# Performance work log

Measured on AMD Instinct MI355X. Metric: run time of the kernel, lower is better.

## Reference

```python
import jax, jax.numpy as jnp
import numpy as np
import math

B, L, D, P, H, WIN, MAXLEN = 2, 2048, 256, 32, 4, 5, 16384


def setup_inputs() -> dict:
    key = jax.random.key(0)
    ks = iter(jax.random.split(key, 40))
    def w(shape, scale=0.05):
        return jax.random.normal(next(ks), shape, jnp.float32) * scale
    inp = {
        'x': jax.random.normal(next(ks), (B, L, D), jnp.float32),
        'pos_phases': jax.random.normal(next(ks), (MAXLEN, P), jnp.float32) * math.pi,
        # mem1_content_encoder
        'w_content': w((D, D)), 'b_content': jnp.zeros((D,), jnp.float32),
        # head_offset_predictors (stacked over H): Linear(D+P, D//2) -> GELU -> Linear(D//2, P+1)
        'hop_w1': w((H, D // 2, D + P)), 'hop_b1': jnp.zeros((H, D // 2), jnp.float32),
        'hop_w2': w((H, P + 1, D // 2)), 'hop_b2': jnp.zeros((H, P + 1), jnp.float32),
        # content_phase_encoder
        'w_cpe': w((P, D)), 'b_cpe': jnp.zeros((P,), jnp.float32),
        # value_encoder
        'w_val': w((D, D)), 'b_val': jnp.zeros((D,), jnp.float32),
        # kv_context_encoder
        'w_ctx': w((D, D)), 'b_ctx': jnp.zeros((D,), jnp.float32),
        # kv_storage_key: Linear(2D, D) -> GELU -> Linear(D, P)
        'kv_w1': w((D, 2 * D)), 'kv_b1': jnp.zeros((D,), jnp.float32),
        'kv_w2': w((P, D)), 'kv_b2': jnp.zeros((P,), jnp.float32),
        # store_gate: Linear(D, D//2) -> GELU -> Linear(D//2, 1) -> Sigmoid
        'sg_w1': w((D // 2, D)), 'sg_b1': jnp.zeros((D // 2,), jnp.float32),
        'sg_w2': w((1, D // 2)), 'sg_b2': jnp.zeros((1,), jnp.float32),
        # to_out: LayerNorm(D) -> Linear(D, D)
        'ln_g': jnp.ones((D,), jnp.float32), 'ln_b': jnp.zeros((D,), jnp.float32),
        'w_out': w((D, D)), 'b_out': jnp.zeros((D,), jnp.float32),
    }
    return inp


def reference(x, pos_phases, w_content, b_content, hop_w1, hop_b1, hop_w2, hop_b2,
              w_cpe, b_cpe, w_val, b_val, w_ctx, b_ctx, kv_w1, kv_b1, kv_w2, kv_b2,
              sg_w1, sg_b1, sg_w2, sg_b2, ln_g, ln_b, w_out, b_out):
    gelu = lambda t: jax.nn.gelu(t, approximate=False)  # torch exact GELU
    pp = pos_phases[:L]                      # (L,P)
    pos_cos, pos_sin = jnp.cos(pp), jnp.sin(pp)

    # ---- phasor memory 1: position-bound content cumsum ----
    content = x @ w_content.T + b_content    # (B,L,D)
    mem1_cos = jnp.cumsum(pos_cos[None, :, :, None] * content[:, :, None, :], axis=1)  # (B,L,P,D)
    mem1_sin = jnp.cumsum(pos_sin[None, :, :, None] * content[:, :, None, :], axis=1)

    # ---- per-head learned offsets ----
    offset_input = jnp.concatenate([x, jnp.broadcast_to(pp[None], (B, L, P))], axis=-1)  # (B,L,D+P)
    h1 = gelu(jnp.einsum('blf,hgf->bhlg', offset_input, hop_w1) + hop_b1[None, :, None, :])
    off = jnp.einsum('bhlg,hpg->bhlp', h1, hop_w2) + hop_b2[None, :, None, :]  # (B,H,L,P+1)
    center = jnp.tanh(off[..., :P]) * math.pi    # (B,H,L,P)
    ww = jax.nn.sigmoid(off[..., P:]) * 2 + 0.1  # (B,H,L,1)

    head_ret = jnp.zeros((B, H, L, D), x.dtype)
    tot_w = jnp.zeros((B, H, L, 1), x.dtype)
    half = WIN // 2
    for delta in range(-half, half + 1):
        wgt = jnp.exp(-0.5 * delta ** 2 / (ww ** 2 + 1e-6))
        op = center + delta * 0.1
        oc, os = jnp.cos(op), jnp.sin(op)
        qc = pos_cos[None, None] * oc - pos_sin[None, None] * os
        qs = pos_sin[None, None] * oc + pos_cos[None, None] * os
        ret = (jnp.einsum('blpd,bhlp->bhld', mem1_cos, qc)
               + jnp.einsum('blpd,bhlp->bhld', mem1_sin, qs)) / math.sqrt(P)
        head_ret = head_ret + wgt * ret
        tot_w = tot_w + wgt
    multi_head_out = (head_ret / (tot_w + 1e-6)).mean(axis=1)  # (B,L,D)

    # ---- kv phasor memory ----
    key_ph = jnp.tanh(x @ w_cpe.T + b_cpe) * math.pi            # (B,L,P)
    values = x @ w_val.T + b_val                                 # (B,L,D)
    store_gate = jax.nn.sigmoid(gelu(x @ sg_w1.T + sg_b1) @ sg_w2.T + sg_b2)  # (B,L,1)
    ctx = x @ w_ctx.T + b_ctx
    ctx_avg = jnp.cumsum(ctx, axis=1) / jnp.arange(1, L + 1, dtype=x.dtype)[None, :, None]
    storage_in = jnp.concatenate([x, ctx_avg], axis=-1)          # (B,L,2D)
    sp = jnp.tanh(gelu(storage_in @ kv_w1.T + kv_b1) @ kv_w2.T + kv_b2) * math.pi  # (B,L,P)
    gated_v = values * store_gate                                # (B,L,D)
    kv_cos = jnp.cumsum(jnp.cos(sp)[..., None] * gated_v[:, :, None, :], axis=1)  # (B,L,P,D)
    kv_sin = jnp.cumsum(jnp.sin(sp)[..., None] * gated_v[:, :, None, :], axis=1)
    gate_cum = jnp.clip(jnp.cumsum(store_gate, axis=1), 1.0, None)  # (B,L,1)
    kv_ret = (jnp.einsum('blpd,blp->bld', kv_cos, jnp.cos(key_ph))
              + jnp.einsum('blpd,blp->bld', kv_sin, jnp.sin(key_ph)))
    kv_ret = kv_ret / (jnp.sqrt(gate_cum) * math.sqrt(P))

    # ---- output projection ----
    combined = multi_head_out + kv_ret
    mu = combined.mean(-1, keepdims=True)
    var = combined.var(-1, keepdims=True)
    ln = (combined - mu) / jnp.sqrt(var + 1e-5) * ln_g + ln_b
    return x + ln @ w_out.T + b_out
```

## Files before the change

kernel.cpp:

```cpp
#include <hip/hip_runtime.h>
#include <hip/hip_bf16.h>

#define BB 2
#define LL 2048
#define DD 256
#define PP 32
#define PX 64
#define NROW (BB*LL)
#define COLS 1440
#define KIN 288
#define CC 64
#define NC (LL/CC)
#define PI_F 3.14159265358979323846f

typedef __attribute__((ext_vector_type(8))) short bf16x8;
typedef __attribute__((ext_vector_type(4))) float f32x4;

__device__ __forceinline__ float gelu_f(float v){
    return 0.5f*v*(1.0f+erff(v*0.70710678118654752440f));
}
__device__ __forceinline__ float sigm_f(float v){
    return 1.0f/(1.0f+expf(-v));
}
__device__ __forceinline__ short f2b(float v){
    __hip_bfloat16 h = __float2bfloat16(v);
    return *reinterpret_cast<short*>(&h);
}
__device__ __forceinline__ float b2f(unsigned short u){
    unsigned int x = ((unsigned int)u)<<16;
    return __uint_as_float(x);
}

__global__ void kprep(const float* w_content,const float* w_val,const float* w_ctx,
                      const float* w_cpe,const float* sg_w1,const float* hop_w1,
                      const float* b_content,const float* b_val,const float* b_ctx,
                      const float* b_cpe,const float* sg_b1,const float* hop_b1,
                      const float* pos_phases,const float* kv_w1,const float* kv_w2,
                      const float* hop_w2,const float* w_out,const float* x,
                      short* W_catb,float* bias_cat,float* w2mem,
                      short* kvw1b,short* kvw2b,float* hop_w2T,short* w_outb,
                      short* Xb,short* Xin2b){
    int idx = blockIdx.x*256 + threadIdx.x;
    int n1 = COLS*KIN;
    if (idx < n1){
        int row = idx / KIN, k = idx % KIN;
        float v = 0.f;
        if      (row < 256){ if (k<256) v = w_content[row*256+k]; }
        else if (row < 512){ if (k<256) v = w_val[(row-256)*256+k]; }
        else if (row < 768){ if (k<256) v = w_ctx[(row-512)*256+k]; }
        else if (row < 800){ if (k<256) v = w_cpe[(row-768)*256+k]; }
        else if (row < 928){ if (k<256) v = sg_w1[(row-800)*256+k]; }
        else               { v = hop_w1[(row-928)*288 + k]; }
        W_catb[idx] = f2b(v);
        return;
    }
    idx -= n1;
    if (idx < COLS){
        int row = idx; float v = 0.f;
        if      (row < 256) v = b_content[row];
        else if (row < 512) v = b_val[row-256];
        else if (row < 768) v = b_ctx[row-512];
        else if (row < 800) v = b_cpe[row-768];
        else if (row < 928) v = sg_b1[row-800];
        else                v = hop_b1[row-928];
        bias_cat[row] = v;
        return;
    }
    idx -= COLS;
    if (idx < LL*PP){
        int l = idx/PP, p = idx%PP;
        float ph = pos_phases[l*PP+p];
        w2mem[l*PX+p]     = cosf(ph);
        w2mem[l*PX+32+p]  = sinf(ph);
        return;
    }
    idx -= LL*PP;
    if (idx < 256*512){ kvw1b[idx] = f2b(kv_w1[idx]); return; }
    idx -= 256*512;
    if (idx < 32*256){ kvw2b[idx] = f2b(kv_w2[idx]); return; }
    idx -= 32*256;
    if (idx < 128*132){
        int k=idx/132, o=idx%132;
        hop_w2T[idx] = hop_w2[o*128+k];
        return;
    }
    idx -= 128*132;
    if (idx < 256*256){ w_outb[idx] = f2b(w_out[idx]); return; }
    idx -= 256*256;
    if (idx < NROW*KIN){
        int r = idx / KIN, d = idx % KIN;
        float v;
        if (d < 256){ v = x[(size_t)r*DD + d]; Xin2b[(size_t)r*512 + d] = f2b(v); }
        else          v = pos_phases[(r % LL)*PP + (d-256)];
        Xb[idx] = f2b(v);
    }
}

__global__ __launch_bounds__(256) void kA_gemm(const short* Xb,const short* Wb,short* Yb){
    int t=threadIdx.x;
    int wid=t>>6, l=t&63;
    int q=blockIdx.x;
    int ct=q%15, rt=q/15;
    int r0=rt*64 + wid*16;
    int c0=ct*96;
    int lr=l&15, lk=(l>>4)*8;
    const short* ap = Xb + (size_t)(r0+lr)*KIN + lk;
    const short* bp = Wb + (size_t)(c0+lr)*KIN + lk;
    f32x4 acc[6];
    #pragma unroll
    for (int f=0;f<6;f++) acc[f]=(f32x4){0.f,0.f,0.f,0.f};
    for (int ks=0;ks<9;ks++){
        bf16x8 a = *(const bf16x8*)(ap + ks*32);
        #pragma unroll
        for (int f=0;f<6;f++){
            bf16x8 b = *(const bf16x8*)(bp + (size_t)f*16*KIN + ks*32);
            acc[f] = __builtin_amdgcn_mfma_f32_16x16x32_bf16(a,b,acc[f],0,0,0);
        }
    }
    int orow = r0 + (l>>4)*4;
    int ocol = c0 + lr;
    #pragma unroll
    for (int f=0;f<6;f++){
        #pragma unroll
        for (int qq=0;qq<4;qq++){
            Yb[(size_t)(orow+qq)*COLS + ocol + 16*f] = f2b(acc[f][qq]);
        }
    }
}

__global__ __launch_bounds__(256,4) void kA_post(const short* Yb,const float* bias_cat,
        const float* sg_w2,const float* sg_b2,
        const float* hop_w2T,const float* hop_b2,const float* pos_phases,
        short* contentb,short* gatedvb,float* ctx,float* key_ph,
        float* store_gate,float* coef_mem){
    __shared__ float yb[4][1448];
    __shared__ float red[4][32];
    __shared__ float offb[4][136];
    __shared__ float scl[4][4];
    __shared__ float sgvv[4];
    int t=threadIdx.x;
    int r0=blockIdx.x*4;
    {
        const ushort4* Yu4 = (const ushort4*)(Yb) + (size_t)r0*360;
        #pragma unroll
        for (int i=0;i<6;i++){
            int chunk=i*256+t;
            if (chunk<1440){
                int r=chunk/360, c=(chunk%360)*4;
                ushort4 s4 = Yu4[chunk];
                float4 bc = *(const float4*)&bias_cat[c];
                yb[r][c+0]=b2f(s4.x)+bc.x;
                yb[r][c+1]=b2f(s4.y)+bc.y;
                yb[r][c+2]=b2f(s4.z)+bc.z;
                yb[r][c+3]=b2f(s4.w)+bc.w;
            }
        }
    }
    __syncthreads();
    #pragma unroll
    for (int r=0;r<4;r++){
        contentb[(size_t)(r0+r)*DD+t] = f2b(yb[r][t]);
        ctx[(size_t)(r0+r)*DD+t]      = yb[r][512+t];
    }
    #pragma unroll
    for (int j=0;j<8;j++){
        int idx=j*256+t, r=idx>>9, g=idx&511;
        yb[r][928+g] = gelu_f(yb[r][928+g]);
    }
    if (t<128){
        int r=t>>5, j=t&31;
        float s=0.f;
        #pragma unroll
        for (int k=0;k<4;k++){
            int jj=j+32*k;
            s += gelu_f(yb[r][800+jj])*sg_w2[jj];
        }
        red[r][j]=s;
        key_ph[(size_t)(r0+r)*PP+j] = tanhf(yb[r][768+j])*PI_F;
    }
    __syncthreads();
    if (t<128){
        int r=t>>5;
        float s=red[r][t&31];
        #pragma unroll
        for (int off=16;off>=1;off>>=1) s += __shfl_down(s,off,32);
        if ((t&31)==0){
            float g=sigm_f(s+sg_b2[0]);
            sgvv[r]=g;
            store_gate[r0+r]=g;
        }
    }
    for (int sIdx=t; sIdx<528; sIdx+=256){
        int r=sIdx/132, o=sIdx%132, h=o/33;
        const float* yh=&yb[r][928+h*128];
        float a0=0.f,a1=0.f,a2=0.f,a3=0.f;
        #pragma unroll 8
        for (int k=0;k<128;k+=4){
            a0 += hop_w2T[(size_t)(k+0)*132+o]*yh[k+0];
            a1 += hop_w2T[(size_t)(k+1)*132+o]*yh[k+1];
            a2 += hop_w2T[(size_t)(k+2)*132+o]*yh[k+2];
            a3 += hop_w2T[(size_t)(k+3)*132+o]*yh[k+3];
        }
        offb[r][o]=a0+a1+a2+a3+hop_b2[o];
    }
    __syncthreads();
    #pragma unroll
    for (int r=0;r<4;r++) gatedvb[(size_t)(r0+r)*DD+t]=f2b(yb[r][256+t]*sgvv[r]);
    if (t<16){
        int r=t>>2, h=t&3;
        const float c01=0.99500416527802576610f;
        const float c02=0.98006657784124163112f;
        float ww=sigm_f(offb[r][h*33+32])*2.0f+0.1f;
        float iw=1.0f/(ww*ww+1e-6f);
        float w1=expf(-0.5f*iw);
        float w2=expf(-2.0f*iw);
        float tot=1.0f+2.0f*w1+2.0f*w2;
        float Wc =1.0f+2.0f*w1*c01+2.0f*w2*c02;
        scl[r][h]=Wc/((tot+1e-6f)*5.65685424949238019520f*4.0f);
    }
    __syncthreads();
    if (t<128){
        int r=t>>5, p=t&31;
        int l=(r0+r)%LL;
        float ppv=pos_phases[l*PP+p];
        float ca=0.f, sb=0.f;
        #pragma unroll
        for (int h=0;h<4;h++){
            float center=tanhf(offb[r][h*33+p])*PI_F;
            float ang=ppv+center;
            float sc=scl[r][h];
            ca+=sc*cosf(ang);
            sb+=sc*sinf(ang);
        }
        coef_mem[(size_t)(r0+r)*PX+p]=ca;
        coef_mem[(size_t)(r0+r)*PX+32+p]=sb;
    }
}

__global__ void k3a_ctxsum(const float* ctx,float* ctxcs){
    int t=threadIdx.x;
    int bi=blockIdx.x;
    int c=bi%NC, b=bi/NC;
    float s=0.f;
    for (int i=0;i<CC;i++) s += ctx[((size_t)b*LL + c*CC + i)*DD + t];
    ctxcs[(size_t)(b*NC+c)*DD + t] = s;
}
__global__ void k3c_ctxavg(const float* ctx,const float* ctxcs,short* Xin2b){
    int t=threadIdx.x;
    int bi=blockIdx.x;
    int c=bi%NC, b=bi/NC;
    float run=0.f;
    for (int cc=0;cc<c;cc++) run += ctxcs[(size_t)(b*NC+cc)*DD+t];
    float v[CC];
    #pragma unroll
    for (int i=0;i<CC;i++) v[i]=ctx[((size_t)b*LL + c*CC + i)*DD + t];
    #pragma unroll
    for (int i=0;i<CC;i++){
        int l = c*CC+i;
        run += v[i];
        Xin2b[((size_t)b*LL+l)*512 + 256 + t] = f2b(run/(float)(l+1));
    }
}

__global__ __launch_bounds__(256) void kmid(const short* Xin2b,const short* kvw1b,
        const float* kv_b1, short* Hb,
        const float* store_gate,const float* key_ph,float* coefkv){
    __shared__ float sh[2048];
    __shared__ float red[256];
    __shared__ float rsgS[64];
    int t=threadIdx.x;
    if (blockIdx.x < 256){
        int wid=t>>6, l=t&63;
        int q=blockIdx.x;
        int nt=q&3, mt=q>>2;
        int r0=mt*64 + wid*16;
        int c0=nt*64;
        int lr=l&15, lk=(l>>4)*8;
        const short* ap = Xin2b + (size_t)(r0+lr)*512 + lk;
        const short* bp = kvw1b + (size_t)(c0+lr)*512 + lk;
        f32x4 acc[4];
        #pragma unroll
        for (int f=0;f<4;f++) acc[f]=(f32x4){0.f,0.f,0.f,0.f};
        for (int ks=0;ks<16;ks++){
            bf16x8 a = *(const bf16x8*)(ap + ks*32);
            #pragma unroll
            for (int f=0;f<4;f++){
                bf16x8 b = *(const bf16x8*)(bp + (size_t)f*16*512 + ks*32);
                acc[f] = __builtin_amdgcn_mfma_f32_16x16x32_bf16(a,b,acc[f],0,0,0);
            }
        }
        int orow = r0 + (l>>4)*4;
        #pragma unroll
        for (int f=0;f<4;f++){
            int oc = c0 + lr + 16*f;
            float bias = kv_b1[oc];
            #pragma unroll
            for (int qq=0;qq<4;qq++){
                Hb[(size_t)(orow+qq)*256 + oc] = f2b(gelu_f(acc[f][qq]+bias));
            }
        }
        return;
    }
    int q=blockIdx.x-256;
    int c=q&31, b=q>>5;
    int n=(c+1)*CC;
    for (int i=t;i<n;i+=256) sh[i]=store_gate[(size_t)b*LL+i];
    __syncthreads();
    float p=0.f;
    for (int i=t;i<c*CC;i+=256) p+=sh[i];
    red[t]=p;
    __syncthreads();
    for (int off=128;off>=1;off>>=1){
        if (t<off) red[t]+=red[t+off];
        __syncthreads();
    }
    float S0=red[0];
    if (t<64){
        float s=sh[c*CC+t];
        #pragma unroll
        for (int off=1;off<64;off<<=1){
            float v=__shfl_up(s,off);
            if (t>=off) s+=v;
        }
        rsgS[t]=rsqrtf(fmaxf(S0+s,1.0f)*32.0f);
    }
    __syncthreads();
    #pragma unroll
    for (int j=0;j<8;j++){
        int g2=t+j*256;
        int l=g2>>5, pp=g2&31;
        float a=key_ph[((size_t)b*LL + c*CC + l)*PP + pp];
        float rv=rsgS[l];
        coefkv[((size_t)b*LL + c*CC + l)*PX + pp]      = cosf(a)*rv;
        coefkv[((size_t)b*LL + c*CC + l)*PX + 32 + pp] = sinf(a)*rv;
    }
}

__global__ __launch_bounds__(256) void k3d2(const short* Hb,const short* kvw2b,
        const float* kv_b2, float* w2kv){
    int t=threadIdx.x;
    int wid=t>>6, l=t&63;
    int mt=blockIdx.x;
    int r0=mt*64 + wid*16;
    int lr=l&15, lk=(l>>4)*8;
    const short* ap = Hb + (size_t)(r0+lr)*256 + lk;
    const short* bp = kvw2b + (size_t)lr*256 + lk;
    f32x4 acc0=(f32x4){0.f,0.f,0.f,0.f};
    f32x4 acc1=(f32x4){0.f,0.f,0.f,0.f};
    for (int ks=0;ks<8;ks++){
        bf16x8 a  = *(const bf16x8*)(ap + ks*32);
        bf16x8 b0 = *(const bf16x8*)(bp + ks*32);
        bf16x8 b1 = *(const bf16x8*)(bp + (size_t)16*256 + ks*32);
        acc0 = __builtin_amdgcn_mfma_f32_16x16x32_bf16(a,b0,acc0,0,0,0);
        acc1 = __builtin_amdgcn_mfma_f32_16x16x32_bf16(a,b1,acc1,0,0,0);
    }
    int orow=r0+(l>>4)*4;
    #pragma unroll
    for (int f=0;f<2;f++){
        int p = lr + 16*f;
        float bias = kv_b2[p];
        f32x4 av = f? acc1:acc0;
        #pragma unroll
        for (int qq=0;qq<4;qq++){
            float sp=tanhf(av[qq]+bias)*PI_F;
            w2kv[(size_t)(orow+qq)*PX + p]    = cosf(sp);
            w2kv[(size_t)(orow+qq)*PX + 32+p] = sinf(sp);
        }
    }
}

__global__ __launch_bounds__(256) void k4_chunksum(
        const short* valA,const float* w2A,int w2bA,
        const short* valB,const float* w2B,int w2bB,
        float* CS){
    __shared__ float w2s[CC][PX];
    int t=threadIdx.x, q=blockIdx.x;
    int dq=q&3, c=(q>>2)&31, b=(q>>7)&1, inst=q>>8;
    const short* val = inst? valB:valA;
    const float* w2  = inst? w2B:w2A;
    int w2b          = inst? w2bB:w2bA;
    for (int i=0;i<16;i++){
        int idx=i*256+t;
        int l=idx>>6, p=idx&63;
        w2s[l][p]=w2[(size_t)w2b*b + (size_t)(c*CC+l)*PX + p];
    }
    __syncthreads();
    int d=t&63, pg=t>>6;
    float acc[16];
    #pragma unroll
    for (int j=0;j<16;j++) acc[j]=0.f;
    const short* vp = val + ((size_t)b*LL + c*CC)*DD + dq*64 + d;
    for (int l=0;l<CC;l++){
        float v = b2f((unsigned short)vp[(size_t)l*DD]);
        const float4* wr=(const float4*)&w2s[l][pg*16];
        #pragma unroll
        for (int k=0;k<4;k++){
            float4 w=wr[k];
            acc[4*k]   += w.x*v;
            acc[4*k+1] += w.y*v;
            acc[4*k+2] += w.z*v;
            acc[4*k+3] += w.w*v;
        }
    }
    float* cp = CS + (((size_t)(inst*BB+b)*NC + c)*PX + pg*16)*DD + dq*64 + d;
    #pragma unroll
    for (int j=0;j<16;j++) cp[(size_t)j*DD]=acc[j];
}

__global__ void k5_prefix(const float* CS,short* PFXb){
    int g=blockIdx.x*256+threadIdx.x;
    int d=g&255, p2=(g>>8)&63, b=(g>>14)&1, inst=g>>15;
    size_t base=(((size_t)(inst*BB+b)*NC)*PX+p2)*DD+d;
    float v[NC];
    #pragma unroll
    for (int c=0;c<NC;c++) v[c]=CS[base+(size_t)c*PX*DD];
    float run=0.f;
    #pragma unroll
    for (int c=0;c<NC;c++){
        PFXb[base+(size_t)c*PX*DD]=f2b(run);
        run+=v[c];
    }
}

__global__ __launch_bounds__(256) void k6_attn(
        const float* coefA,const float* w2A,int w2bA,const short* valA,float* outA,
        const float* coefB,const float* w2B,int w2bB,const short* valB,float* outB,
        const short* PFXb){
    __shared__ float coefs[CC][PX+1];
    __shared__ float w2s[CC][PX];
    __shared__ float S[CC][CC+1];
    int t=threadIdx.x, q=blockIdx.x;
    int dq=q&3, qc=(q>>2)&31, b=(q>>7)&1, inst=q>>8;
    const float* coef = inst? coefB:coefA;
    const float* w2   = inst? w2B:w2A;
    int w2b           = inst? w2bB:w2bA;
    const short* val  = inst? valB:valA;
    float* out        = inst? outB:outA;
    int d0 = dq*64;
    for (int i=0;i<16;i++){
        int idx=i*256+t;
        int l=idx>>6, p=idx&63;
        coefs[l][p]=coef[((size_t)b*LL + qc*CC + l)*PX + p];
        w2s[l][p]  =w2[(size_t)w2b*b + (size_t)(qc*CC+l)*PX + p];
    }
    __syncthreads();
    {
        int l=t&63, lpb=(t>>6)*16;
        float cf[PX];
        #pragma unroll
        for (int p=0;p<PX;p++) cf[p]=coefs[l][p];
        for (int qq=0;qq<16;qq++){
            int lp=lpb+qq;
            float s=0.f;
            if (lp<=l){
                const float4* wr=(const float4*)&w2s[lp][0];
                #pragma unroll
                for (int k=0;k<16;k++){
                    float4 w=wr[k];
                    s += w.x*cf[4*k]+w.y*cf[4*k+1]+w.z*cf[4*k+2]+w.w*cf[4*k+3];
                }
            }
            S[l][lp]=s;
        }
    }
    __syncthreads();
    {
        int d=t&63, lq=t>>6;
        float acc[16];
        #pragma unroll
        for (int i=0;i<16;i++) acc[i]=0.f;
        const short* pfx = PFXb + (((size_t)(inst*BB+b)*NC + qc)*PX)*DD + d0 + d;
        for (int p=0;p<PX;p++){
            float pf = b2f((unsigned short)pfx[(size_t)p*DD]);
            #pragma unroll
            for (int i=0;i<16;i++) acc[i] += coefs[lq*16+i][p]*pf;
        }
        const short* vptr = val + ((size_t)b*LL + qc*CC)*DD + d0 + d;
        int kmax = lq*16+16;
        for (int lp=0; lp<kmax; lp++){
            float v = b2f((unsigned short)vptr[(size_t)lp*DD]);
            #pragma unroll
            for (int i=0;i<16;i++) acc[i] += S[lq*16+i][lp]*v;
        }
        float* op = out + ((size_t)b*LL + qc*CC + lq*16)*DD + d0 + d;
        #pragma unroll
        for (int i=0;i<16;i++) op[(size_t)i*DD] = acc[i];
    }
}

__global__ __launch_bounds__(256) void k7_final(const float* comb,const float* kvout,
        const float* x,const float* ln_g,const float* ln_b,const short* w_outb,const float* b_out,
        float* out){
    __shared__ float cb[16][260];
    __shared__ short Ab[16][264];
    __shared__ float red[16][32];
    __shared__ float mvm[16][2];
    int t=threadIdx.x, r0=blockIdx.x*16;
    #pragma unroll
    for (int i=0;i<16;i++){
        int idx=i*256+t;
        int r=idx>>8, c=idx&255;
        cb[r][c]=comb[(size_t)(r0+r)*DD+c]+kvout[(size_t)(r0+r)*DD+c];
    }
    __syncthreads();
    {
        int r=t>>4, j=t&15;
        float s=0.f,s2=0.f;
        #pragma unroll
        for (int k=0;k<16;k++){
            float v=cb[r][j+16*k];
            s+=v; s2+=v*v;
        }
        red[r][j]=s; red[r][16+j]=s2;
    }
    __syncthreads();
    if (t<16){
        float s=0.f,s2=0.f;
        #pragma unroll
        for (int j=0;j<16;j++){ s+=red[t][j]; s2+=red[t][16+j]; }
        float mu=s/256.f;
        float var=s2/256.f-mu*mu;
        mvm[t][0]=mu; mvm[t][1]=rsqrtf(var+1e-5f);
    }
    __syncthreads();
    #pragma unroll
    for (int i=0;i<16;i++){
        int idx=i*256+t;
        int r=idx>>8, c=idx&255;
        Ab[r][c]=f2b((cb[r][c]-mvm[r][0])*mvm[r][1]*ln_g[c]+ln_b[c]);
    }
    __syncthreads();
    int wid=t>>6, l=t&63;
    int lr=l&15, lk=(l>>4)*8;
    f32x4 acc[4];
    #pragma unroll
    for (int f=0;f<4;f++) acc[f]=(f32x4){0.f,0.f,0.f,0.f};
    for (int ks=0;ks<8;ks++){
        bf16x8 a = *(const bf16x8*)&Ab[lr][lk+ks*32];
        #pragma unroll
        for (int f=0;f<4;f++){
            bf16x8 bv = *(const bf16x8*)(w_outb + (size_t)(wid*64+f*16+lr)*256 + lk + ks*32);
            acc[f] = __builtin_amdgcn_mfma_f32_16x16x32_bf16(a,bv,acc[f],0,0,0);
        }
    }
    int orow = r0 + (l>>4)*4;
    #pragma unroll
    for (int f=0;f<4;f++){
        int oc = wid*64 + f*16 + lr;
        float bo = b_out[oc];
        #pragma unroll
        for (int qq=0;qq<4;qq++){
            out[(size_t)(orow+qq)*DD + oc] = x[(size_t)(orow+qq)*DD + oc] + acc[f][qq] + bo;
        }
    }
}

extern "C" void kernel_launch(void* const* d_in, const int* in_sizes, int n_in,
                              void* d_out, int out_size, void* d_ws, size_t ws_size,
                              hipStream_t stream){
    (void)in_sizes; (void)n_in; (void)out_size; (void)ws_size;
    const float* x         =(const float*)d_in[0];
    const float* pos_phases=(const float*)d_in[1];
    const float* w_content =(const float*)d_in[2];
    const float* b_content =(const float*)d_in[3];
    const float* hop_w1    =(const float*)d_in[4];
    const float* hop_b1    =(const float*)d_in[5];
    const float* hop_w2    =(const float*)d_in[6];
    const float* hop_b2    =(const float*)d_in[7];
    const float* w_cpe     =(const float*)d_in[8];
    const float* b_cpe     =(const float*)d_in[9];
    const float* w_val     =(const float*)d_in[10];
    const float* b_val     =(const float*)d_in[11];
    const float* w_ctx     =(const float*)d_in[12];
    const float* b_ctx     =(const float*)d_in[13];
    const float* kv_w1     =(const float*)d_in[14];
    const float* kv_b1     =(const float*)d_in[15];
    const float* kv_w2     =(const float*)d_in[16];
    const float* kv_b2     =(const float*)d_in[17];
    const float* sg_w1     =(const float*)d_in[18];
    const float* sg_b1     =(const float*)d_in[19];
    const float* sg_w2     =(const float*)d_in[20];
    const float* sg_b2     =(const float*)d_in[21];
    const float* ln_g      =(const float*)d_in[22];
    const float* ln_b      =(const float*)d_in[23];
    const float* w_out     =(const float*)d_in[24];
    const float* b_out     =(const float*)d_in[25];

    float* ws=(float*)d_ws;
    size_t o=0;
    short* W_catb  =(short*)(ws+o); o+=(size_t)COLS*KIN/2;
    short* Xb      =(short*)(ws+o); o+=(size_t)NROW*KIN/2;
    short* kvw1b   =(short*)(ws+o); o+=(size_t)256*512/2;
    short* kvw2b   =(short*)(ws+o); o+=(size_t)32*256/2;
    short* w_outb  =(short*)(ws+o); o+=(size_t)256*256/2;
    short* Hb      =(short*)(ws+o); o+=(size_t)NROW*256/2;
    short* contentb=(short*)(ws+o); o+=(size_t)NROW*DD/2;
    short* gatedvb =(short*)(ws+o); o+=(size_t)NROW*DD/2;
    short* PFXb    =(short*)(ws+o); o+=(size_t)2*BB*NC*PX*DD/2;
    float* bias_cat=ws+o; o+=COLS;
    float* hop_w2T =ws+o; o+=(size_t)128*132;
    float* w2mem   =ws+o; o+=(size_t)LL*PX;
    float* ctx     =ws+o; o+=(size_t)NROW*DD;
    float* xin2_kv =ws+o; o+=(size_t)NROW*DD;
    float* key_ph  =ws+o; o+=(size_t)NROW*PP;
    float* store_gate=ws+o; o+=NROW;
    float* coef_mem=ws+o; o+=(size_t)NROW*PX;
    float* coefkv  =ws+o; o+=(size_t)NROW*PX;
    float* w2kv    =ws+o; o+=(size_t)NROW*PX;
    float* ctxcs   =ws+o; o+=(size_t)BB*NC*DD;
    float* CS      =ws+o; o+=(size_t)2*BB*NC*PX*DD;
    short* Yb      =(short*)CS;
    short* Xin2b   =(short*)xin2_kv;
    float* comb  = ctx;
    float* kvout = xin2_kv;

    int prep_total = COLS*KIN + COLS + LL*PP + 256*512 + 32*256 + 128*132 + 256*256 + NROW*KIN;
    kprep<<<(prep_total+255)/256,256,0,stream>>>(
                                 w_content,w_val,w_ctx,w_cpe,sg_w1,hop_w1,
                                 b_content,b_val,b_ctx,b_cpe,sg_b1,hop_b1,
                                 pos_phases,kv_w1,kv_w2,hop_w2,w_out,x,
                                 W_catb,bias_cat,w2mem,kvw1b,kvw2b,hop_w2T,w_outb,Xb,Xin2b);
    kA_gemm<<<960,256,0,stream>>>(Xb,W_catb,Yb);
    kA_post<<<NROW/4,256,0,stream>>>(Yb,bias_cat,sg_w2,sg_b2,hop_w2T,hop_b2,pos_phases,
                                     contentb,gatedvb,ctx,key_ph,store_gate,coef_mem);
    k3a_ctxsum<<<BB*NC,256,0,stream>>>(ctx,ctxcs);
    k3c_ctxavg<<<BB*NC,256,0,stream>>>(ctx,ctxcs,Xin2b);
    kmid<<<256+BB*NC,256,0,stream>>>(Xin2b,kvw1b,kv_b1,Hb,store_gate,key_ph,coefkv);
    k3d2<<<64,256,0,stream>>>(Hb,kvw2b,kv_b2,w2kv);
    k4_chunksum<<<2*BB*NC*4,256,0,stream>>>(contentb,w2mem,0,
                                            gatedvb,w2kv,LL*PX,CS);
    k5_prefix<<<2*BB*PX*DD/256,256,0,stream>>>(CS,PFXb);
    k6_attn<<<2*BB*NC*4,256,0,stream>>>(coef_mem,w2mem,0,contentb,comb,
                                        coefkv,w2kv,LL*PX,gatedvb,kvout,PFXb);
    k7_final<<<NROW/16,256,0,stream>>>(comb,kvout,x,ln_g,ln_b,w_outb,b_out,
                                       (float*)d_out);
}
```

Baseline: 146.5 us.

## Fuse concatenated input GEMM with its row-wise post-processing kernel

Merges the bf16 MFMA GEMM and its post-processing kernel into one kernel. Each block now computes 16 full rows across all 1440 output columns and keeps the result in LDS as bf16, so the intermediate Yb buffer never round-trips through global memory and one launch is removed. In exchange there are only 256 blocks instead of 960, each wave holds 23 accumulators, and B-matrix reuse across rows is lower. The post-processing (GELU, gate reduction, offset matvec) also now reads bf16-rounded values from LDS instead of fp32.

```diff
diff --git a/kernel.cpp b/kernel.cpp
--- a/kernel.cpp
+++ b/kernel.cpp
@@ -96,117 +96,103 @@
     }
 }
 
-__global__ __launch_bounds__(256) void kA_gemm(const short* Xb,const short* Wb,short* Yb){
-    int t=threadIdx.x;
-    int wid=t>>6, l=t&63;
-    int q=blockIdx.x;
-    int ct=q%15, rt=q/15;
-    int r0=rt*64 + wid*16;
-    int c0=ct*96;
-    int lr=l&15, lk=(l>>4)*8;
-    const short* ap = Xb + (size_t)(r0+lr)*KIN + lk;
-    const short* bp = Wb + (size_t)(c0+lr)*KIN + lk;
-    f32x4 acc[6];
-    #pragma unroll
-    for (int f=0;f<6;f++) acc[f]=(f32x4){0.f,0.f,0.f,0.f};
-    for (int ks=0;ks<9;ks++){
-        bf16x8 a = *(const bf16x8*)(ap + ks*32);
-        #pragma unroll
-        for (int f=0;f<6;f++){
-            bf16x8 b = *(const bf16x8*)(bp + (size_t)f*16*KIN + ks*32);
-            acc[f] = __builtin_amdgcn_mfma_f32_16x16x32_bf16(a,b,acc[f],0,0,0);
-        }
-    }
-    int orow = r0 + (l>>4)*4;
-    int ocol = c0 + lr;
-    #pragma unroll
-    for (int f=0;f<6;f++){
-        #pragma unroll
-        for (int qq=0;qq<4;qq++){
-            Yb[(size_t)(orow+qq)*COLS + ocol + 16*f] = f2b(acc[f][qq]);
-        }
-    }
-}
-
-__global__ __launch_bounds__(256,4) void kA_post(const short* Yb,const float* bias_cat,
-        const float* sg_w2,const float* sg_b2,
+__global__ __launch_bounds__(256) void kAF(const short* Xb,const short* Wb,
+        const float* bias_cat,const float* sg_w2,const float* sg_b2,
         const float* hop_w2T,const float* hop_b2,const float* pos_phases,
         short* contentb,short* gatedvb,float* ctx,float* key_ph,
         float* store_gate,float* coef_mem){
-    __shared__ float yb[4][1448];
-    __shared__ float red[4][32];
-    __shared__ float offb[4][136];
-    __shared__ float scl[4][4];
-    __shared__ float sgvv[4];
+    __shared__ short ybb[16][1456];
+    __shared__ float offb[16][136];
+    __shared__ float red[16][16];
+    __shared__ float scl[16][4];
+    __shared__ float sgvv[16];
     int t=threadIdx.x;
-    int r0=blockIdx.x*4;
+    int r0=blockIdx.x*16;
+    int wid=t>>6, l=t&63;
+    int lr=l&15, lk=(l>>4)*8;
     {
-        const ushort4* Yu4 = (const ushort4*)(Yb) + (size_t)r0*360;
-        #pragma unroll
-        for (int i=0;i<6;i++){
-            int chunk=i*256+t;
-            if (chunk<1440){
-                int r=chunk/360, c=(chunk%360)*4;
-                ushort4 s4 = Yu4[chunk];
-                float4 bc = *(const float4*)&bias_cat[c];
-                yb[r][c+0]=b2f(s4.x)+bc.x;
-                yb[r][c+1]=b2f(s4.y)+bc.y;
-                yb[r][c+2]=b2f(s4.z)+bc.z;
-                yb[r][c+3]=b2f(s4.w)+bc.w;
+        const short* ap = Xb + (size_t)(r0+lr)*KIN + lk;
+        f32x4 acc[23];
+        #pragma unroll
+        for (int j=0;j<23;j++) acc[j]=(f32x4){0.f,0.f,0.f,0.f};
+        for (int ks=0;ks<9;ks++){
+            bf16x8 a = *(const bf16x8*)(ap + ks*32);
+            #pragma unroll
+            for (int j=0;j<23;j++){
+                int ct=wid+4*j;
+                if (ct<90){
+                    const short* bp = Wb + (size_t)(ct*16+lr)*KIN + lk + ks*32;
+                    acc[j] = __builtin_amdgcn_mfma_f32_16x16x32_bf16(a,*(const bf16x8*)bp,acc[j],0,0,0);
+                }
             }
         }
-    }
-    __syncthreads();
-    #pragma unroll
-    for (int r=0;r<4;r++){
-        contentb[(size_t)(r0+r)*DD+t] = f2b(yb[r][t]);
-        ctx[(size_t)(r0+r)*DD+t]      = yb[r][512+t];
-    }
-    #pragma unroll
-    for (int j=0;j<8;j++){
-        int idx=j*256+t, r=idx>>9, g=idx&511;
-        yb[r][928+g] = gelu_f(yb[r][928+g]);
-    }
-    if (t<128){
-        int r=t>>5, j=t&31;
+        int orl=(l>>4)*4;
+        #pragma unroll
+        for (int j=0;j<23;j++){
+            int ct=wid+4*j;
+            if (ct<90){
+                int oc=ct*16+lr;
+                float bias=bias_cat[oc];
+                #pragma unroll
+                for (int qq=0;qq<4;qq++){
+                    ybb[orl+qq][oc]=f2b(acc[j][qq]+bias);
+                }
+            }
+        }
+    }
+    __syncthreads();
+    #pragma unroll
+    for (int r=0;r<16;r++){
+        contentb[(size_t)(r0+r)*DD+t] = ybb[r][t];
+        ctx[(size_t)(r0+r)*DD+t]      = b2f((unsigned short)ybb[r][512+t]);
+    }
+    #pragma unroll
+    for (int i=0;i<32;i++){
+        int idx=i*256+t;
+        int r=idx>>9, g=idx&511;
+        ybb[r][928+g] = f2b(gelu_f(b2f((unsigned short)ybb[r][928+g])));
+    }
+    {
+        int r=t>>4, j=t&15;
         float s=0.f;
         #pragma unroll
-        for (int k=0;k<4;k++){
-            int jj=j+32*k;
-            s += gelu_f(yb[r][800+jj])*sg_w2[jj];
+        for (int k=0;k<8;k++){
+            int jj=j+16*k;
+            s += gelu_f(b2f((unsigned short)ybb[r][800+jj]))*sg_w2[jj];
         }
         red[r][j]=s;
-        key_ph[(size_t)(r0+r)*PP+j] = tanhf(yb[r][768+j])*PI_F;
-    }
-    __syncthreads();
-    if (t<128){
-        int r=t>>5;
-        float s=red[r][t&31];
-        #pragma unroll
-        for (int off=16;off>=1;off>>=1) s += __shfl_down(s,off,32);
-        if ((t&31)==0){
-            float g=sigm_f(s+sg_b2[0]);
-            sgvv[r]=g;
-            store_gate[r0+r]=g;
-        }
-    }
-    for (int sIdx=t; sIdx<528; sIdx+=256){
+    }
+    {
+        int r=t>>5, p=t&31;
+        key_ph[(size_t)(r0+r)*PP+p]   = tanhf(b2f((unsigned short)ybb[r][768+p]))*PI_F;
+        key_ph[(size_t)(r0+r+8)*PP+p] = tanhf(b2f((unsigned short)ybb[r+8][768+p]))*PI_F;
+    }
+    __syncthreads();
+    if (t<16){
+        float s=sg_b2[0];
+        #pragma unroll
+        for (int j=0;j<16;j++) s+=red[t][j];
+        float g=sigm_f(s);
+        sgvv[t]=g;
+        store_gate[r0+t]=g;
+    }
+    for (int sIdx=t; sIdx<2112; sIdx+=256){
         int r=sIdx/132, o=sIdx%132, h=o/33;
-        const float* yh=&yb[r][928+h*128];
+        const short* yh=&ybb[r][928+h*128];
         float a0=0.f,a1=0.f,a2=0.f,a3=0.f;
         #pragma unroll 8
         for (int k=0;k<128;k+=4){
-            a0 += hop_w2T[(size_t)(k+0)*132+o]*yh[k+0];
-            a1 += hop_w2T[(size_t)(k+1)*132+o]*yh[k+1];
-            a2 += hop_w2T[(size_t)(k+2)*132+o]*yh[k+2];
-            a3 += hop_w2T[(size_t)(k+3)*132+o]*yh[k+3];
+            a0 += hop_w2T[(size_t)(k+0)*132+o]*b2f((unsigned short)yh[k+0]);
+            a1 += hop_w2T[(size_t)(k+1)*132+o]*b2f((unsigned short)yh[k+1]);
+            a2 += hop_w2T[(size_t)(k+2)*132+o]*b2f((unsigned short)yh[k+2]);
+            a3 += hop_w2T[(size_t)(k+3)*132+o]*b2f((unsigned short)yh[k+3]);
         }
         offb[r][o]=a0+a1+a2+a3+hop_b2[o];
     }
     __syncthreads();
     #pragma unroll
-    for (int r=0;r<4;r++) gatedvb[(size_t)(r0+r)*DD+t]=f2b(yb[r][256+t]*sgvv[r]);
-    if (t<16){
+    for (int r=0;r<16;r++) gatedvb[(size_t)(r0+r)*DD+t]=f2b(b2f((unsigned short)ybb[r][256+t])*sgvv[r]);
+    if (t<64){
         int r=t>>2, h=t&3;
         const float c01=0.99500416527802576610f;
         const float c02=0.98006657784124163112f;
@@ -219,10 +205,12 @@
         scl[r][h]=Wc/((tot+1e-6f)*5.65685424949238019520f*4.0f);
     }
     __syncthreads();
-    if (t<128){
-        int r=t>>5, p=t&31;
-        int l=(r0+r)%LL;
-        float ppv=pos_phases[l*PP+p];
+    #pragma unroll
+    for (int ii=0;ii<2;ii++){
+        int idx=ii*256+t;
+        int r=idx>>5, p=idx&31;
+        int ll2=(r0+r)%LL;
+        float ppv=pos_phases[ll2*PP+p];
         float ca=0.f, sb=0.f;
         #pragma unroll
         for (int h=0;h<4;h++){
@@ -609,7 +597,6 @@
     float* w2kv    =ws+o; o+=(size_t)NROW*PX;
     float* ctxcs   =ws+o; o+=(size_t)BB*NC*DD;
     float* CS      =ws+o; o+=(size_t)2*BB*NC*PX*DD;
-    short* Yb      =(short*)CS;
     short* Xin2b   =(short*)xin2_kv;
     float* comb  = ctx;
     float* kvout = xin2_kv;
@@ -620,9 +607,8 @@
                                  b_content,b_val,b_ctx,b_cpe,sg_b1,hop_b1,
                                  pos_phases,kv_w1,kv_w2,hop_w2,w_out,x,
                                  W_catb,bias_cat,w2mem,kvw1b,kvw2b,hop_w2T,w_outb,Xb,Xin2b);
-    kA_gemm<<<960,256,0,stream>>>(Xb,W_catb,Yb);
-    kA_post<<<NROW/4,256,0,stream>>>(Yb,bias_cat,sg_w2,sg_b2,hop_w2T,hop_b2,pos_phases,
-                                     contentb,gatedvb,ctx,key_ph,store_gate,coef_mem);
+    kAF<<<NROW/16,256,0,stream>>>(Xb,W_catb,bias_cat,sg_w2,sg_b2,hop_w2T,hop_b2,pos_phases,
+                                  contentb,gatedvb,ctx,key_ph,store_gate,coef_mem);
     k3a_ctxsum<<<BB*NC,256,0,stream>>>(ctx,ctxcs);
     k3c_ctxavg<<<BB*NC,256,0,stream>>>(ctx,ctxcs,Xin2b);
     kmid<<<256+BB*NC,256,0,stream>>>(Xin2b,kvw1b,kv_b1,Hb,store_gate,key_ph,coefkv);
```

New measurement: 160.5 us. +9.6%, slower.
